# Kernel tuning notes

Hardware: AMD Instinct MI355X
Metric: run time of the kernel (lower is better)

The kernel has to match this reference:

```python
import jax, jax.numpy as jnp
import numpy as np

B, T, N, H, L, KS = 8, 1024, 64, 8, 2, 3  # batch, seq_len, num_features(=graph n), heads, blocks, Cheb order
D1 = 64  # tq MLP hidden (hardcoded 64 in original)
EPS = 1e-6


def setup_inputs() -> dict:
    key = jax.random.key(0)
    ks = jax.random.split(key, 30)
    def nrm(k, shp, sc=0.05):
        return jax.random.normal(k, shp, dtype=jnp.float32) * sc
    return {
        "inputs": jax.random.normal(ks[0], (B, T, N), dtype=jnp.float32),
        "pos_emb": nrm(ks[1], (T, N)),
        "K3": nrm(ks[2], (N, KS, N), 0.1),  # Chebyshev kernel Lk reshaped [n, Ks, n] (constant)
        "qw": nrm(ks[3], (L, H, KS)), "qb": nrm(ks[4], (L, H)),
        "kw": nrm(ks[5], (L, H, KS)), "kb": nrm(ks[6], (L, H)),
        "vw": nrm(ks[7], (L, H, KS)), "vb": nrm(ks[8], (L, H)),
        "tqW1": nrm(ks[9], (L, H, T, D1)), "tqb1": nrm(ks[10], (L, H, D1)),
        "tqW2": nrm(ks[11], (L, H, D1, D1)), "tqb2": nrm(ks[12], (L, H, D1)),
        "tqW3": nrm(ks[13], (L, H, D1, 2)), "tqb3": nrm(ks[14], (L, H, 2)),
        "Wlt": nrm(ks[15], (L, H * N, N)),
        "ln1g": jnp.ones((L, N), jnp.float32), "ln1b": jnp.zeros((L, N), jnp.float32),
        "ln2g": jnp.ones((L, N), jnp.float32), "ln2b": jnp.zeros((L, N), jnp.float32),
        "sclw": nrm(ks[16], (L, KS)), "sclb": nrm(ks[17], (L,)),
        "elW": nrm(ks[18], (L, N, N)), "elb": nrm(ks[19], (L, N)),
        "fW1": nrm(ks[20], (N, 32)), "fb1": nrm(ks[21], (32,)),
        "fW2": nrm(ks[22], (32, 1)), "fb2": nrm(ks[23], (1,)),
    }


def _ln(x, g, b):
    m = jnp.mean(x, axis=-1, keepdims=True)
    v = jnp.mean((x - m) ** 2, axis=-1, keepdims=True)
    return (x - m) * jax.lax.rsqrt(v + EPS) * g + b


def _head_gconv(x, K3, ws, bs):
    # SpatialConvLayer (c_in=c_out=1) per head: relu(sum_k ws[h,k]*(x @ L_k) + bs[h] + x)
    g = jnp.einsum('btn,nkm,hk->bhtm', x, K3, ws) + bs[None, :, None, None]
    return jax.nn.relu(g + x[:, None])  # [B,H,T,N]


def reference(inputs, pos_emb, K3, qw, qb, kw, kb, vw, vb, tqW1, tqb1, tqW2, tqb2,
              tqW3, tqb3, Wlt, ln1g, ln1b, ln2g, ln2b, sclw, sclb, elW, elb,
              fW1, fb1, fW2, fb2):
    x = inputs + pos_emb  # position embedding layer
    for l in range(L):
        xq = _head_gconv(x, K3, qw[l], qb[l])
        xk = _head_gconv(x, K3, kw[l], kb[l])
        xv = _head_gconv(x, K3, vw[l], vb[l])
        # s_a[b,t,s] = sum_n xk[b,t,n] * xq[b,s,n], scaled by 1/num_features
        s = jnp.einsum('bhtn,bhsn->bhts', xk, xq) / N
        sft = jax.nn.softmax(s, axis=-1)
        # talking-quantity gate: MLP over rows of transposed softmax matrix
        p = jnp.swapaxes(sft, -1, -2)  # [B,H,T,T]
        h1 = jax.nn.relu(jnp.einsum('bhts,hsd->bhtd', p, tqW1[l]) + tqb1[l][None, :, None, :])
        h2 = jax.nn.relu(jnp.einsum('bhtd,hde->bhte', h1, tqW2[l]) + tqb2[l][None, :, None, :])
        g = jax.nn.softmax(jnp.einsum('bhtd,hde->bhte', h2, tqW3[l]) + tqb3[l][None, :, None, :], axis=-1)  # [B,H,T,2]
        auv = jnp.einsum('bhts,bhsn->bhtn', sft, xv)
        ho = g[..., 0:1] * auv + g[..., 1:2] * xv  # gated mix, [B,H,T,N]
        a_x = jnp.transpose(ho, (0, 2, 1, 3)).reshape(B, T, H * N)  # head concat
        out1 = _ln(x + a_x @ Wlt[l], ln1g[l], ln1b[l])  # dropout omitted (inference)
        gc = jnp.einsum('btn,nkm,k->btm', out1, K3, sclw[l]) + sclb[l]
        ffn = jax.nn.relu(gc + out1)  # SpatialConvLayer residual relu
        ffn = ffn @ elW[l] + elb[l]
        x = _ln(out1 + ffn, ln2g[l], ln2b[l])
    pooled = jnp.mean(x, axis=1)  # GlobalAveragePooling1D
    h = jax.nn.relu(pooled @ fW1 + fb1)
    return h @ fW2 + fb2  # [B,1]
```

## Files before the change

### kernel.cpp

```cpp
#include <hip/hip_runtime.h>

typedef __attribute__((ext_vector_type(8))) short short8;
typedef __attribute__((ext_vector_type(4))) float f32x4;

#define BB 8
#define TT 1024
#define NN 64
#define HH 8
#define LL 2
#define KSS 3
#define DD1 64
#define EPSV 1e-6f
#define LOG2E 1.4426950408889634f

#define MFMA16(a, b, c) __builtin_amdgcn_mfma_f32_16x16x32_bf16(a, b, c, 0, 0, 0)
#define BAR() __builtin_amdgcn_s_barrier()
#define WAIT_VM6() asm volatile("s_waitcnt vmcnt(6)" ::: "memory")
#define WAIT_VM2() asm volatile("s_waitcnt vmcnt(2)" ::: "memory")
#define WAIT_VM0() asm volatile("s_waitcnt vmcnt(0)" ::: "memory")
#define WAIT_LGKM0() asm volatile("s_waitcnt lgkmcnt(0)" ::: "memory")

__device__ __forceinline__ float exp2_(float x) { return __builtin_amdgcn_exp2f(x); }
__device__ __forceinline__ float log2_(float x) { return __builtin_amdgcn_logf(x); }

__device__ __forceinline__ void split1(float x, ushort& hi, ushort& lo) {
  uint u = __float_as_uint(x);
  hi = (ushort)(u >> 16);
  float hf = __uint_as_float(u & 0xffff0000u);
  lo = (ushort)(__float_as_uint(x - hf) >> 16);
}
__device__ __forceinline__ uint pack2(float a, float b, uint& lo) {
  uint ua = __float_as_uint(a), ub = __float_as_uint(b);
  float ra = __uint_as_float(ua & 0xffff0000u);
  float rb = __uint_as_float(ub & 0xffff0000u);
  lo = (__float_as_uint(a - ra) >> 16) | (__float_as_uint(b - rb) & 0xffff0000u);
  return (ua >> 16) | (ub & 0xffff0000u);
}
__device__ __forceinline__ uint pack2rhu(float a, float b) {
  uint ua = __float_as_uint(a) + 0x8000u;
  uint ub = __float_as_uint(b) + 0x8000u;
  return (ua >> 16) | (ub & 0xffff0000u);
}
__device__ __forceinline__ ushort f2bfr(float x) {
  union { float f; uint u; } v; v.f = x;
  uint r = (v.u + 0x7fffu + ((v.u >> 16) & 1u)) >> 16;
  return (ushort)r;
}
__device__ __forceinline__ float bf2f(ushort b) {
  union { uint u; float f; } v; v.u = ((uint)b) << 16; return v.f;
}

__device__ __forceinline__ void gl2lds16(const ushort* g, ushort* l) {
  __builtin_amdgcn_global_load_lds(
      (const __attribute__((address_space(1))) void*)g,
      (__attribute__((address_space(3))) void*)l, 16, 0, 0);
}
__device__ __forceinline__ void stage_async(ushort* __restrict__ s,
                                            const ushort* __restrict__ g,
                                            int stride, int tid) {
  int w = tid >> 6;
  int sub = (tid & 63) >> 3, c = tid & 7;
#pragma unroll
  for (int i = 0; i < 2; ++i) {
    int rb = (i * 4 + w) * 8;
    gl2lds16(g + (size_t)(rb + sub) * stride + ((c ^ sub) << 3), s + rb * 64);
  }
}
__device__ __forceinline__ short8 frag(const ushort* __restrict__ s, int row, int ch) {
  return *(const short8*)(s + row * 64 + ((ch ^ (row & 7)) << 3));
}
__device__ __forceinline__ void stage_q32(ushort* __restrict__ s,
                                          const ushort* __restrict__ g, int tid) {
  int w = tid >> 6;
  int sub = (tid & 63) >> 3, c = tid & 7;
  int rb = w * 8, r = rb + sub;
  gl2lds16(g + (size_t)r * 64 + ((c ^ (r & 7)) << 3), s + rb * 64);
}
__device__ __forceinline__ void stage_v32(ushort* __restrict__ s,
                                          const ushort* __restrict__ g, int tid) {
  int w = tid >> 6;
  int noff = (tid & 63) >> 2, c = tid & 3;
  int nb = w * 16, n = nb + noff;
  gl2lds16(g + (size_t)n * 1024 + ((c ^ ((n >> 1) & 3)) << 3), s + nb * 32);
}
__device__ __forceinline__ short8 frag32(const ushort* __restrict__ s, int row, int g) {
  return *(const short8*)(s + row * 32 + ((g ^ ((row >> 1) & 3)) << 3));
}


__global__ void k_addpos(const float* __restrict__ in, const float* __restrict__ pe,
                         float* __restrict__ x, int total) {
  int idx = blockIdx.x * 256 + threadIdx.x;
  if (idx < total) {
    int tn = idx & (TT * NN - 1);
    x[idx] = in[idx] + pe[tn];
  }
}

__global__ void k_k3s(const float* __restrict__ K3, const float* __restrict__ sclwl,
                      ushort* __restrict__ dh) {
  int idx = blockIdx.x * 256 + threadIdx.x;
  int n = idx >> 6, m = idx & 63;
  float v = K3[n * 192 + m] * sclwl[0] + K3[n * 192 + 64 + m] * sclwl[1] +
            K3[n * 192 + 128 + m] * sclwl[2];
  dh[m * 64 + n] = f2bfr(v);
}

__global__ __launch_bounds__(256) void k_tsplit(const float* __restrict__ src,
                                                ushort* __restrict__ dh) {
  __shared__ float st[64][65];
  int blk = blockIdx.x;
  int mat = blk >> 4, rt = blk & 15;
  int tid = threadIdx.x;
  size_t sbase = ((size_t)mat * TT + rt * 64) * 64;
#pragma unroll
  for (int i = 0; i < 4; ++i) {
    int idx = tid + i * 256;
    int r = idx >> 4, c4 = idx & 15;
    float4 v = *(const float4*)(src + sbase + r * 64 + c4 * 4);
    st[r][c4 * 4 + 0] = v.x; st[r][c4 * 4 + 1] = v.y;
    st[r][c4 * 4 + 2] = v.z; st[r][c4 * 4 + 3] = v.w;
  }
  __syncthreads();
  size_t obase = (size_t)mat * (64 * (size_t)TT) + rt * 64;
#pragma unroll
  for (int i = 0; i < 2; ++i) {
    int idx = tid + i * 256;
    int n = idx >> 3, c = idx & 7;
    uint hw[4];
#pragma unroll
    for (int j = 0; j < 4; ++j)
      hw[j] = (uint)f2bfr(st[c * 8 + 2 * j][n]) | ((uint)f2bfr(st[c * 8 + 2 * j + 1][n]) << 16);
    *(uint4*)(dh + obase + (size_t)n * TT + c * 8) = make_uint4(hw[0], hw[1], hw[2], hw[3]);
  }
}

__global__ __launch_bounds__(256) void k_tsplitW(const float* __restrict__ Wlt,
                                                 ushort* __restrict__ dh,
                                                 ushort* __restrict__ dl) {
  __shared__ float st[64][65];
  int blk = blockIdx.x;
  int l = blk >> 3, rt = blk & 7;
  int tid = threadIdx.x;
  size_t sbase = ((size_t)l * 512 + rt * 64) * 64;
#pragma unroll
  for (int i = 0; i < 4; ++i) {
    int idx = tid + i * 256;
    int r = idx >> 4, c4 = idx & 15;
    float4 v = *(const float4*)(Wlt + sbase + r * 64 + c4 * 4);
    st[r][c4 * 4 + 0] = v.x; st[r][c4 * 4 + 1] = v.y;
    st[r][c4 * 4 + 2] = v.z; st[r][c4 * 4 + 3] = v.w;
  }
  __syncthreads();
  size_t obase = (size_t)l * 64 * 512 + rt * 64;
#pragma unroll
  for (int i = 0; i < 2; ++i) {
    int idx = tid + i * 256;
    int n = idx >> 3, c = idx & 7;
    uint hw[4], lw[4];
#pragma unroll
    for (int j = 0; j < 4; ++j) hw[j] = pack2(st[c * 8 + 2 * j][n], st[c * 8 + 2 * j + 1][n], lw[j]);
    *(uint4*)(dh + obase + (size_t)n * 512 + c * 8) = make_uint4(hw[0], hw[1], hw[2], hw[3]);
    *(uint4*)(dl + obase + (size_t)n * 512 + c * 8) = make_uint4(lw[0], lw[1], lw[2], lw[3]);
  }
}

__global__ __launch_bounds__(256) void k_tsplitSq(const float* __restrict__ src,
                                                  ushort* __restrict__ dh) {
  __shared__ float st[64][65];
  int mat = blockIdx.x;
  int tid = threadIdx.x;
  size_t sbase = (size_t)mat * 4096;
#pragma unroll
  for (int i = 0; i < 4; ++i) {
    int idx = tid + i * 256;
    int r = idx >> 4, c4 = idx & 15;
    float4 v = *(const float4*)(src + sbase + r * 64 + c4 * 4);
    st[r][c4 * 4 + 0] = v.x; st[r][c4 * 4 + 1] = v.y;
    st[r][c4 * 4 + 2] = v.z; st[r][c4 * 4 + 3] = v.w;
  }
  __syncthreads();
#pragma unroll
  for (int i = 0; i < 2; ++i) {
    int idx = tid + i * 256;
    int d = idx >> 3, c = idx & 7;
    uint hw[4];
#pragma unroll
    for (int j = 0; j < 4; ++j)
      hw[j] = (uint)f2bfr(st[c * 8 + 2 * j][d]) | ((uint)f2bfr(st[c * 8 + 2 * j + 1][d]) << 16);
    *(uint4*)(dh + sbase + (size_t)d * 64 + c * 8) = make_uint4(hw[0], hw[1], hw[2], hw[3]);
  }
}

__global__ __launch_bounds__(256) void k_gconv(
    const float* __restrict__ x, const float* __restrict__ K3,
    const float* __restrict__ qwl, const float* __restrict__ qbl,
    const float* __restrict__ kwl, const float* __restrict__ kbl,
    const float* __restrict__ vwl, const float* __restrict__ vbl,
    ushort* __restrict__ xqh, ushort* __restrict__ xkh, float* __restrict__ xv) {
  __shared__ float sK3[12288];
  __shared__ float sx[4][64];
  int tid = threadIdx.x;
  int w = tid >> 6, lane = tid & 63;
#pragma unroll
  for (int i = 0; i < 12; ++i)
    ((float4*)sK3)[tid + i * 256] = ((const float4*)K3)[tid + i * 256];
  size_t bt = (size_t)blockIdx.x * 4 + w;
  size_t b = bt >> 10, t = bt & 1023;
  float xm = x[bt * 64 + lane];
  sx[w][lane] = xm;
  __syncthreads();
  float a0 = 0.f, a1 = 0.f, a2 = 0.f;
#pragma unroll 8
  for (int n = 0; n < 64; ++n) {
    float xn = sx[w][n];
    a0 = fmaf(xn, sK3[n * 192 + lane], a0);
    a1 = fmaf(xn, sK3[n * 192 + 64 + lane], a1);
    a2 = fmaf(xn, sK3[n * 192 + 128 + lane], a2);
  }
#pragma unroll
  for (int hh = 0; hh < HH; ++hh) {
    size_t off = (((size_t)b * HH + hh) * TT + t) * 64 + lane;
    float q = fmaf(qwl[hh * 3 + 0], a0,
              fmaf(qwl[hh * 3 + 1], a1, fmaf(qwl[hh * 3 + 2], a2, qbl[hh] + xm)));
    q = fmaxf(q, 0.f) * (0.015625f * LOG2E);
    xqh[off] = f2bfr(q);
    float k = fmaf(kwl[hh * 3 + 0], a0,
              fmaf(kwl[hh * 3 + 1], a1, fmaf(kwl[hh * 3 + 2], a2, kbl[hh] + xm)));
    xkh[off] = f2bfr(fmaxf(k, 0.f));
    float v = fmaf(vwl[hh * 3 + 0], a0,
              fmaf(vwl[hh * 3 + 1], a1, fmaf(vwl[hh * 3 + 2], a2, vbl[hh] + xm)));
    xv[off] = fmaxf(v, 0.f);
  }
}

__global__ __launch_bounds__(256) void k_attn(
    const ushort* __restrict__ xkh, const ushort* __restrict__ xqh,
    const ushort* __restrict__ xvTh,
    float* __restrict__ auv0, float* __restrict__ auv1,
    float* __restrict__ ls0, float* __restrict__ ls1) {
  __shared__ ushort sQh[4096];
  __shared__ ushort sVh[4096];
  __shared__ ushort sPh[2048];
  int tid = threadIdx.x;
  int lane = tid & 63, w = tid >> 6;
  int l15 = lane & 15, g = lane >> 4;
  int nb = gridDim.x, chunk = nb >> 3, bid = blockIdx.x;
  int blk = (bid & 7) * chunk + (bid >> 3);
  int bh = blk >> 5, t0 = ((blk >> 1) & 15) << 6, half = blk & 1;
  size_t bhTT = (size_t)bh * TT;
  size_t ubase = (size_t)(half << 9);
  int trow = 16 * w + l15, psw = (trow >> 1) & 3;

  stage_async(sQh, xkh + (bhTT + t0) * NN, 64, tid);
  WAIT_VM0();
  BAR();
  short8 fKh[2];
#pragma unroll
  for (int ks = 0; ks < 2; ++ks) fKh[ks] = frag(sQh, trow, g + 4 * ks);
  WAIT_LGKM0();
  BAR();
  stage_q32(sQh, xqh + (bhTT + ubase) * NN, tid);
  stage_v32(sVh, xvTh + bhTT * NN + ubase, tid);
  stage_q32(sQh + 2048, xqh + (bhTT + ubase + 32) * NN, tid);
  stage_v32(sVh + 2048, xvTh + bhTT * NN + ubase + 32, tid);

  float lsum = 0.f;
  f32x4 O[4];
#pragma unroll
  for (int ct = 0; ct < 4; ++ct)
#pragma unroll
    for (int r = 0; r < 4; ++r) O[ct][r] = 0.f;

  for (int ut = 0; ut < 16; ++ut) {
    int cur = ut & 1;
    if (ut < 15) WAIT_VM2(); else WAIT_VM0();
    BAR();
    const ushort* cQh = sQh + cur * 2048;
    const ushort* cVh = sVh + cur * 2048;

    __builtin_amdgcn_s_setprio(1);
    f32x4 S[2];
#pragma unroll
    for (int rt = 0; rt < 2; ++rt) {
      f32x4 a = {0.f, 0.f, 0.f, 0.f};
#pragma unroll
      for (int ks = 0; ks < 2; ++ks)
        a = MFMA16(frag(cQh, 16 * rt + l15, g + 4 * ks), fKh[ks], a);
      S[rt] = a;
    }
    __builtin_amdgcn_s_setprio(0);

    uint2 ph[2];
#pragma unroll
    for (int rt = 0; rt < 2; ++rt) {
      float p0 = exp2_(S[rt][0]), p1 = exp2_(S[rt][1]);
      float p2 = exp2_(S[rt][2]), p3 = exp2_(S[rt][3]);
      lsum += (p0 + p1) + (p2 + p3);
      ph[rt].x = pack2rhu(p0, p1);
      ph[rt].y = pack2rhu(p2, p3);
    }
#pragma unroll
    for (int rt = 0; rt < 2; ++rt) {
      int ch = 2 * rt + (g >> 1);
      int off = trow * 32 + ((ch ^ psw) << 3) + ((g & 1) << 2);
      *(uint2*)(sPh + off) = ph[rt];
    }
    WAIT_LGKM0();
    __builtin_amdgcn_sched_barrier(0);
    __builtin_amdgcn_s_setprio(1);
    {
      short8 aPh = frag32(sPh, trow, g);
#pragma unroll
      for (int ct = 0; ct < 4; ++ct)
        O[ct] = MFMA16(aPh, frag32(cVh, 16 * ct + l15, g), O[ct]);
    }
    __builtin_amdgcn_s_setprio(0);
    WAIT_LGKM0();
    BAR();
    if (ut < 14) {
      int tn = ut + 2;
      stage_q32(sQh + cur * 2048, xqh + (bhTT + ubase + tn * 32) * NN, tid);
      stage_v32(sVh + cur * 2048, xvTh + bhTT * NN + ubase + tn * 32, tid);
    }
  }
  lsum += __shfl_xor(lsum, 16, 64);
  lsum += __shfl_xor(lsum, 32, 64);
  float* A = half ? auv1 : auv0;
  float* L = half ? ls1 : ls0;
#pragma unroll
  for (int r = 0; r < 4; ++r) {
    size_t row = (bhTT + t0 + 16 * w + 4 * g + r) * NN;
#pragma unroll
    for (int ct = 0; ct < 4; ++ct) A[row + 16 * ct + l15] = O[ct][r];
  }
  if (g == 0) L[bhTT + t0 + trow] = lsum;
}

__global__ __launch_bounds__(256, 4) void k_h1g(
    const ushort* __restrict__ xkh, const ushort* __restrict__ xqh,
    const ushort* __restrict__ w1Th,
    const float* __restrict__ ls0, const float* __restrict__ ls1,
    const float* __restrict__ b1, const ushort* __restrict__ w2Th,
    const float* __restrict__ b2l, const float* __restrict__ W3l,
    const float* __restrict__ b3l,
    const float* __restrict__ auv0, const float* __restrict__ auv1,
    const float* __restrict__ xv, ushort* __restrict__ hoh,
    ushort* __restrict__ hol) {
  __shared__ ushort sKh[4096];
  __shared__ ushort sWh[4096];
  __shared__ ushort sPh[2048];
  __shared__ ushort sW2[4096];
  __shared__ float sL[1024];
  __shared__ float sIl[1024];
  int tid = threadIdx.x;
  int lane = tid & 63, w = tid >> 6;
  int l15 = lane & 15, g = lane >> 4;
  int nb = gridDim.x, chunk = nb >> 3, bid = blockIdx.x;
  int blk = (bid & 7) * chunk + (bid >> 3);
  int bh = blk >> 4, h = bh & (HH - 1), a0 = (blk & 15) << 6;
  size_t bhTT = (size_t)bh * TT;
  size_t wbase = (size_t)h * NN * TT;
  int arow = 16 * w + l15, psw = (arow >> 1) & 3;

  stage_async(sKh, xqh + (bhTT + a0) * NN, 64, tid);
  stage_async(sW2, w2Th + (size_t)h * 4096, 64, tid);
  WAIT_VM0();
  BAR();
  short8 fQh[2];
#pragma unroll
  for (int ks = 0; ks < 2; ++ks) fQh[ks] = frag(sKh, arow, g + 4 * ks);
#pragma unroll
  for (int i = 0; i < 4; ++i) {
    int idx = tid + i * 256;
    float l = ls0[bhTT + idx] + ls1[bhTT + idx];
    sL[idx] = log2_(l);
    sIl[idx] = 1.0f / l;
  }
  WAIT_LGKM0();
  BAR();
  stage_q32(sKh, xkh + bhTT * NN, tid);
  stage_v32(sWh, w1Th + wbase, tid);
  stage_q32(sKh + 2048, xkh + (bhTT + 32) * NN, tid);
  stage_v32(sWh + 2048, w1Th + wbase + 32, tid);

  f32x4 acc[4];
#pragma unroll
  for (int ct = 0; ct < 4; ++ct)
#pragma unroll
    for (int r = 0; r < 4; ++r) acc[ct][r] = 0.f;

  for (int tt = 0; tt < 32; ++tt) {
    int cur = tt & 1;
    if (tt < 31) WAIT_VM2(); else WAIT_VM0();
    BAR();
    const ushort* cKh = sKh + cur * 2048;
    const ushort* cWh = sWh + cur * 2048;

    __builtin_amdgcn_s_setprio(1);
    f32x4 S[2];
#pragma unroll
    for (int rt = 0; rt < 2; ++rt) {
      f32x4 a = {0.f, 0.f, 0.f, 0.f};
#pragma unroll
      for (int ks = 0; ks < 2; ++ks)
        a = MFMA16(frag(cKh, 16 * rt + l15, g + 4 * ks), fQh[ks], a);
      S[rt] = a;
    }
    __builtin_amdgcn_s_setprio(0);

    uint2 ph[2];
#pragma unroll
    for (int rt = 0; rt < 2; ++rt) {
      f32x4 lv = *(const f32x4*)(sL + tt * 32 + 16 * rt + 4 * g);
      float p0 = exp2_(S[rt][0] - lv[0]);
      float p1 = exp2_(S[rt][1] - lv[1]);
      float p2 = exp2_(S[rt][2] - lv[2]);
      float p3 = exp2_(S[rt][3] - lv[3]);
      ph[rt].x = pack2rhu(p0, p1);
      ph[rt].y = pack2rhu(p2, p3);
    }
#pragma unroll
    for (int rt = 0; rt < 2; ++rt) {
      int ch = 2 * rt + (g >> 1);
      int off = arow * 32 + ((ch ^ psw) << 3) + ((g & 1) << 2);
      *(uint2*)(sPh + off) = ph[rt];
    }
    WAIT_LGKM0();
    __builtin_amdgcn_sched_barrier(0);
    __builtin_amdgcn_s_setprio(1);
    {
      short8 aPh = frag32(sPh, arow, g);
#pragma unroll
      for (int ct = 0; ct < 4; ++ct)
        acc[ct] = MFMA16(aPh, frag32(cWh, 16 * ct + l15, g), acc[ct]);
    }
    __builtin_amdgcn_s_setprio(0);
    WAIT_LGKM0();
    BAR();
    if (tt < 30) {
      int tn = tt + 2;
      stage_q32(sKh + cur * 2048, xkh + (bhTT + tn * 32) * NN, tid);
      stage_v32(sWh + cur * 2048, w1Th + wbase + tn * 32, tid);
    }
  }
#pragma unroll
  for (int ct = 0; ct < 4; ++ct) {
    float bb = b1[h * 64 + 16 * ct + l15];
    int cch = 2 * ct + (l15 >> 3), cin = l15 & 7;
#pragma unroll
    for (int r = 0; r < 4; ++r) {
      int row = 16 * w + 4 * g + r;
      float hv = fmaxf(acc[ct][r] + bb, 0.f);
      sWh[row * 64 + ((cch ^ (row & 7)) << 3) + cin] = f2bfr(hv);
    }
  }
  WAIT_LGKM0();
  BAR();
  f32x4 acc2[4];
#pragma unroll
  for (int rt = 0; rt < 4; ++rt)
#pragma unroll
    for (int r = 0; r < 4; ++r) acc2[rt][r] = 0.f;
#pragma unroll
  for (int ks = 0; ks < 2; ++ks) {
    short8 bB = frag(sW2, 16 * w + l15, g + 4 * ks);
#pragma unroll
    for (int rt = 0; rt < 4; ++rt)
      acc2[rt] = MFMA16(frag(sWh, 16 * rt + l15, g + 4 * ks), bB, acc2[rt]);
  }
  int col = 16 * w + l15;
  float b2c = b2l[h * 64 + col];
  float w30 = W3l[h * 128 + col * 2 + 0];
  float w31 = W3l[h * 128 + col * 2 + 1];
  float* sredf = sL;
  float* sgf = sL + 512;
#pragma unroll
  for (int rt = 0; rt < 4; ++rt)
#pragma unroll
    for (int r = 0; r < 4; ++r) {
      float v = fmaxf(acc2[rt][r] + b2c, 0.f);
      float z0 = v * w30, z1 = v * w31;
#pragma unroll
      for (int mm = 1; mm < 16; mm <<= 1) {
        z0 += __shfl_xor(z0, mm, 64);
        z1 += __shfl_xor(z1, mm, 64);
      }
      if (l15 == 0) {
        int row = 16 * rt + 4 * g + r;
        sredf[row * 4 + w] = z0;
        sredf[256 + row * 4 + w] = z1;
      }
    }
  __syncthreads();
  if (tid < 64) {
    float z0 = sredf[tid * 4] + sredf[tid * 4 + 1] + sredf[tid * 4 + 2] +
               sredf[tid * 4 + 3] + b3l[h * 2 + 0];
    float z1 = sredf[256 + tid * 4] + sredf[256 + tid * 4 + 1] +
               sredf[256 + tid * 4 + 2] + sredf[256 + tid * 4 + 3] + b3l[h * 2 + 1];
    float g0 = 1.0f / (1.0f + __expf(z1 - z0));
    sgf[tid * 2] = g0 * sIl[a0 + tid];
    sgf[tid * 2 + 1] = 1.0f - g0;
  }
  __syncthreads();
#pragma unroll
  for (int rr = 0; rr < 16; ++rr) {
    int row = 16 * w + rr;
    size_t off = (bhTT + a0 + row) * 64 + lane;
    float o = auv0[off] + auv1[off];
    float ho = sgf[row * 2] * o + sgf[row * 2 + 1] * xv[off];
    ushort hb, lb;
    split1(ho, hb, lb);
    hoh[off] = hb;
    hol[off] = lb;
  }
}

__global__ __launch_bounds__(256, 2) void k_mrgf(
    float* __restrict__ x, const ushort* __restrict__ hoh,
    const ushort* __restrict__ hol, const ushort* __restrict__ wth,
    const ushort* __restrict__ wtl, const float* __restrict__ g1l,
    const float* __restrict__ b1l, const float* __restrict__ sclb_l,
    const ushort* __restrict__ k3sTh, const ushort* __restrict__ elWTh,
    const float* __restrict__ elbl, const float* __restrict__ g2l,
    const float* __restrict__ b2l) {
  __shared__ ushort sAh[2][2048], sAl[2][2048], sBh[2][4096], sBl[2][4096];
  __shared__ float sred[2][32][4];
  __shared__ float sfin[32][2];
  int tid = threadIdx.x;
  int lane = tid & 63, w = tid >> 6;
  int l15 = lane & 15, g = lane >> 4;
  int blk = blockIdx.x;
  int b = blk >> 5, t0 = (blk & 31) << 5;

  {
    size_t ab0 = (((size_t)b * HH + 0) * TT + t0) * NN;
    size_t ab1 = (((size_t)b * HH + 1) * TT + t0) * NN;
    stage_q32(sAh[0], hoh + ab0, tid);
    stage_q32(sAl[0], hol + ab0, tid);
    stage_async(sBh[0], wth, 512, tid);
    stage_async(sBl[0], wtl, 512, tid);
    stage_q32(sAh[1], hoh + ab1, tid);
    stage_q32(sAl[1], hol + ab1, tid);
    stage_async(sBh[1], wth + 64, 512, tid);
    stage_async(sBl[1], wtl + 64, 512, tid);
  }

  f32x4 acc[2];
#pragma unroll
  for (int rt = 0; rt < 2; ++rt)
#pragma unroll
    for (int r = 0; r < 4; ++r) acc[rt][r] = 0.f;

  for (int h = 0; h < 8; ++h) {
    int cur = h & 1;
    if (h < 7) WAIT_VM6(); else WAIT_VM0();
    BAR();
    __builtin_amdgcn_s_setprio(1);
#pragma unroll
    for (int ks = 0; ks < 2; ++ks) {
      short8 bBh = frag(sBh[cur], 16 * w + l15, g + 4 * ks);
      short8 bBl = frag(sBl[cur], 16 * w + l15, g + 4 * ks);
#pragma unroll
      for (int rt = 0; rt < 2; ++rt) {
        short8 aAh = frag(sAh[cur], 16 * rt + l15, g + 4 * ks);
        short8 aAl = frag(sAl[cur], 16 * rt + l15, g + 4 * ks);
        acc[rt] = MFMA16(aAh, bBh, acc[rt]);
        acc[rt] = MFMA16(aAh, bBl, acc[rt]);
        acc[rt] = MFMA16(aAl, bBh, acc[rt]);
      }
    }
    __builtin_amdgcn_s_setprio(0);
    WAIT_LGKM0();
    BAR();
    if (h < 6) {
      int hn = h + 2;
      size_t ab = (((size_t)b * HH + hn) * TT + t0) * NN;
      stage_q32(sAh[cur], hoh + ab, tid);
      stage_q32(sAl[cur], hol + ab, tid);
      stage_async(sBh[cur], wth + hn * 64, 512, tid);
      stage_async(sBl[cur], wtl + hn * 64, 512, tid);
    }
  }
  stage_async(sBh[0], k3sTh, 64, tid);
  stage_async(sBl[0], elWTh, 64, tid);
  int mcol = 16 * w + l15;
  float vv[2][4];
#pragma unroll
  for (int rt = 0; rt < 2; ++rt)
#pragma unroll
    for (int r = 0; r < 4; ++r) {
      int row = 16 * rt + 4 * g + r;
      vv[rt][r] = acc[rt][r] + x[((size_t)b * TT + t0 + row) * 64 + mcol];
    }
#pragma unroll
  for (int rt = 0; rt < 2; ++rt)
#pragma unroll
    for (int r = 0; r < 4; ++r) {
      float s1 = vv[rt][r], s2 = vv[rt][r] * vv[rt][r];
#pragma unroll
      for (int mm = 1; mm < 16; mm <<= 1) {
        s1 += __shfl_xor(s1, mm, 64);
        s2 += __shfl_xor(s2, mm, 64);
      }
      if (l15 == 0) {
        int row = 16 * rt + 4 * g + r;
        sred[0][row][w] = s1;
        sred[1][row][w] = s2;
      }
    }
  __syncthreads();
  if (tid < 32) {
    float a1 = sred[0][tid][0] + sred[0][tid][1] + sred[0][tid][2] + sred[0][tid][3];
    float a2 = sred[1][tid][0] + sred[1][tid][1] + sred[1][tid][2] + sred[1][tid][3];
    float mean = a1 * (1.0f / 64.0f);
    float var = a2 * (1.0f / 64.0f) - mean * mean;
    sfin[tid][0] = mean;
    sfin[tid][1] = rsqrtf(var + EPSV);
  }
  __syncthreads();
  float gg = g1l[mcol], bb1 = b1l[mcol];
  float val[2][4];
  ushort* sH = sAh[0];
  ushort* sHl = sAl[0];
  int cch = mcol >> 3, cin = mcol & 7;
#pragma unroll
  for (int rt = 0; rt < 2; ++rt)
#pragma unroll
    for (int r = 0; r < 4; ++r) {
      int row = 16 * rt + 4 * g + r;
      float v = (vv[rt][r] - sfin[row][0]) * sfin[row][1] * gg + bb1;
      val[rt][r] = v;
      ushort hb, lb;
      split1(v, hb, lb);
      int a = row * 64 + ((cch ^ (row & 7)) << 3) + cin;
      sH[a] = hb;
      sHl[a] = lb;
    }
  WAIT_VM0();
  WAIT_LGKM0();
  BAR();
  f32x4 acc3[2];
#pragma unroll
  for (int rt = 0; rt < 2; ++rt)
#pragma unroll
    for (int r = 0; r < 4; ++r) acc3[rt][r] = 0.f;
#pragma unroll
  for (int ks = 0; ks < 2; ++ks) {
    short8 bB = frag(sBh[0], mcol, g + 4 * ks);
#pragma unroll
    for (int rt = 0; rt < 2; ++rt) {
      acc3[rt] = MFMA16(frag(sH, 16 * rt + l15, g + 4 * ks), bB, acc3[rt]);
      acc3[rt] = MFMA16(frag(sHl, 16 * rt + l15, g + 4 * ks), bB, acc3[rt]);
    }
  }
  WAIT_LGKM0();
  BAR();
  float sclb = sclb_l[0];
#pragma unroll
  for (int rt = 0; rt < 2; ++rt)
#pragma unroll
    for (int r = 0; r < 4; ++r) {
      int row = 16 * rt + 4 * g + r;
      float f1 = fmaxf(acc3[rt][r] + sclb + val[rt][r], 0.f);
      ushort hb, lb;
      split1(f1, hb, lb);
      int a = row * 64 + ((cch ^ (row & 7)) << 3) + cin;
      sH[a] = hb;
      sHl[a] = lb;
    }
  WAIT_LGKM0();
  BAR();
  f32x4 acc4[2];
#pragma unroll
  for (int rt = 0; rt < 2; ++rt)
#pragma unroll
    for (int r = 0; r < 4; ++r) acc4[rt][r] = 0.f;
#pragma unroll
  for (int ks = 0; ks < 2; ++ks) {
    short8 bB = frag(sBl[0], mcol, g + 4 * ks);
#pragma unroll
    for (int rt = 0; rt < 2; ++rt) {
      acc4[rt] = MFMA16(frag(sH, 16 * rt + l15, g + 4 * ks), bB, acc4[rt]);
      acc4[rt] = MFMA16(frag(sHl, 16 * rt + l15, g + 4 * ks), bB, acc4[rt]);
    }
  }
  float elb = elbl[mcol];
#pragma unroll
  for (int rt = 0; rt < 2; ++rt)
#pragma unroll
    for (int r = 0; r < 4; ++r) {
      float v = val[rt][r] + acc4[rt][r] + elb;
      vv[rt][r] = v;
      float s1 = v, s2 = v * v;
#pragma unroll
      for (int mm = 1; mm < 16; mm <<= 1) {
        s1 += __shfl_xor(s1, mm, 64);
        s2 += __shfl_xor(s2, mm, 64);
      }
      if (l15 == 0) {
        int row = 16 * rt + 4 * g + r;
        sred[0][row][w] = s1;
        sred[1][row][w] = s2;
      }
    }
  __syncthreads();
  if (tid < 32) {
    float a1 = sred[0][tid][0] + sred[0][tid][1] + sred[0][tid][2] + sred[0][tid][3];
    float a2 = sred[1][tid][0] + sred[1][tid][1] + sred[1][tid][2] + sred[1][tid][3];
    float mean = a1 * (1.0f / 64.0f);
    float var = a2 * (1.0f / 64.0f) - mean * mean;
    sfin[tid][0] = mean;
    sfin[tid][1] = rsqrtf(var + EPSV);
  }
  __syncthreads();
  float g2 = g2l[mcol], bb2 = b2l[mcol];
#pragma unroll
  for (int rt = 0; rt < 2; ++rt)
#pragma unroll
    for (int r = 0; r < 4; ++r) {
      int row = 16 * rt + 4 * g + r;
      x[((size_t)b * TT + t0 + row) * 64 + mcol] =
          (vv[rt][r] - sfin[row][0]) * sfin[row][1] * g2 + bb2;
    }
}

__global__ __launch_bounds__(256) void k_final(
    const float* __restrict__ x, const float* __restrict__ fW1,
    const float* __restrict__ fb1, const float* __restrict__ fW2,
    const float* __restrict__ fb2, float* __restrict__ out) {
  __shared__ float pl[4][64];
  int tid = threadIdx.x;
  int lane = tid & 63, w = tid >> 6;
  size_t b = blockIdx.x;
  float s = 0.f;
  for (int t = 256 * w; t < 256 * w + 256; ++t) s += x[(b * TT + t) * 64 + lane];
  pl[w][lane] = s;
  __syncthreads();
  if (tid < 64) pl[0][tid] = (pl[0][tid] + pl[1][tid] + pl[2][tid] + pl[3][tid]) * (1.0f / TT);
  __syncthreads();
  if (tid < 64) {
    float hv = 0.f;
    if (lane < 32) {
      hv = fb1[lane];
#pragma unroll 8
      for (int n = 0; n < 64; ++n) hv = fmaf(pl[0][n], fW1[n * 32 + lane], hv);
      hv = fmaxf(hv, 0.f) * fW2[lane];
    }
#pragma unroll
    for (int m = 1; m < 64; m <<= 1) hv += __shfl_xor(hv, m, 64);
    if (lane == 0) out[b] = hv + fb2[0];
  }
}

extern "C" void kernel_launch(void* const* d_in, const int* in_sizes, int n_in,
                              void* d_out, int out_size, void* d_ws, size_t ws_size,
                              hipStream_t stream) {
  const float* inputs = (const float*)d_in[0];
  const float* pos_emb = (const float*)d_in[1];
  const float* K3 = (const float*)d_in[2];
  const float* qw = (const float*)d_in[3];
  const float* qb = (const float*)d_in[4];
  const float* kw = (const float*)d_in[5];
  const float* kb = (const float*)d_in[6];
  const float* vw = (const float*)d_in[7];
  const float* vb = (const float*)d_in[8];
  const float* tqW1 = (const float*)d_in[9];
  const float* tqb1 = (const float*)d_in[10];
  const float* tqW2 = (const float*)d_in[11];
  const float* tqb2 = (const float*)d_in[12];
  const float* tqW3 = (const float*)d_in[13];
  const float* tqb3 = (const float*)d_in[14];
  const float* Wlt = (const float*)d_in[15];
  const float* ln1g = (const float*)d_in[16];
  const float* ln1b = (const float*)d_in[17];
  const float* ln2g = (const float*)d_in[18];
  const float* ln2b = (const float*)d_in[19];
  const float* sclw = (const float*)d_in[20];
  const float* sclb = (const float*)d_in[21];
  const float* elW = (const float*)d_in[22];
  const float* elb = (const float*)d_in[23];
  const float* fW1 = (const float*)d_in[24];
  const float* fb1 = (const float*)d_in[25];
  const float* fW2 = (const float*)d_in[26];
  const float* fb2 = (const float*)d_in[27];
  float* out = (float*)d_out;
  float* ws_f = (float*)d_ws;

  const size_t TN = (size_t)TT * NN;
  const size_t HTN = (size_t)HH * TT * NN;
  const size_t W1T_ELEMS = (size_t)LL * HH * NN * TT;
  const size_t WLT_ELEMS = (size_t)LL * 64 * 512;

  ushort* k3sTh = (ushort*)ws_f;
  ushort* w1Th = k3sTh + (size_t)LL * 4096;
  ushort* wth = w1Th + W1T_ELEMS;
  ushort* wtl = wth + WLT_ELEMS;
  ushort* w2Th = wtl + WLT_ELEMS;
  ushort* elWTh = w2Th + (size_t)LL * HH * 4096;
  size_t base_ush = (size_t)LL * 4096 + W1T_ELEMS + 2 * WLT_ELEMS +
                    (size_t)LL * HH * 4096 + (size_t)LL * 4096;
  const size_t base = (base_ush + 1) / 2;

  for (int l = 0; l < LL; ++l)
    k_k3s<<<16, 256, 0, stream>>>(K3, sclw + l * KSS, k3sTh + (size_t)l * 4096);
  k_tsplit<<<LL * HH * 16, 256, 0, stream>>>(tqW1, w1Th);
  k_tsplitW<<<LL * 8, 256, 0, stream>>>(Wlt, wth, wtl);
  k_tsplitSq<<<LL * HH, 256, 0, stream>>>(tqW2, w2Th);
  k_tsplitSq<<<LL, 256, 0, stream>>>(elW, elWTh);

  const size_t per_b = TN + 3 * HTN + 2 * (size_t)HH * TT + (5 * HTN) / 2;
  size_t avail = ws_size / sizeof(float);
  avail = (avail > base) ? avail - base : 0;
  int Bc = (int)(avail / per_b);
  if (Bc > BB) Bc = BB;
  if (Bc < 1) Bc = 1;

  for (int b0 = 0; b0 < BB; b0 += Bc) {
    int bc = (BB - b0 < Bc) ? (BB - b0) : Bc;
    float* x = ws_f + base;
    float* xv = x + (size_t)bc * TN;
    float* auv0 = xv + (size_t)bc * HTN;
    float* auv1 = auv0 + (size_t)bc * HTN;
    float* ls0 = auv1 + (size_t)bc * HTN;
    float* ls1 = ls0 + (size_t)bc * HH * TT;
    ushort* xqh = (ushort*)(ls1 + (size_t)bc * HH * TT);
    ushort* xkh = xqh + (size_t)bc * HTN;
    ushort* xvTh = xkh + (size_t)bc * HTN;
    ushort* hoh = xvTh + (size_t)bc * HTN;
    ushort* hol = hoh + (size_t)bc * HTN;

    int total = bc * (int)TN;
    k_addpos<<<(total + 255) / 256, 256, 0, stream>>>(inputs + (size_t)b0 * TN, pos_emb, x,
                                                      total);
    for (int l = 0; l < LL; ++l) {
      k_gconv<<<bc * TT / 4, 256, 0, stream>>>(x, K3, qw + l * HH * KSS, qb + l * HH,
                                               kw + l * HH * KSS, kb + l * HH,
                                               vw + l * HH * KSS, vb + l * HH,
                                               xqh, xkh, xv);
      k_tsplit<<<bc * HH * 16, 256, 0, stream>>>(xv, xvTh);
      k_attn<<<bc * HH * 32, 256, 0, stream>>>(xkh, xqh, xvTh, auv0, auv1, ls0, ls1);
      k_h1g<<<bc * HH * 16, 256, 0, stream>>>(
          xkh, xqh, w1Th + (size_t)l * HH * NN * TT, ls0, ls1,
          tqb1 + l * HH * DD1, w2Th + (size_t)l * HH * 4096, tqb2 + l * HH * DD1,
          tqW3 + (size_t)l * HH * DD1 * 2, tqb3 + l * HH * 2, auv0, auv1, xv,
          hoh, hol);
      k_mrgf<<<bc * 32, 256, 0, stream>>>(
          x, hoh, hol, wth + (size_t)l * 64 * 512, wtl + (size_t)l * 64 * 512,
          ln1g + l * NN, ln1b + l * NN, sclb + l, k3sTh + (size_t)l * 4096,
          elWTh + (size_t)l * 4096, elb + l * NN, ln2g + l * NN, ln2b + l * NN);
    }
    k_final<<<bc, 256, 0, stream>>>(x, fW1, fb1, fW2, fb2, out + b0);
  }
}
```

Measured before the change: 243.8 us.

## Fuse V transpose into gconv, tile gconv over 32 rows, halve mrgf row tile

The graph-conv kernel now processes 32 time steps per block with register-blocked accumulators. It writes the bf16 transposed V tile directly through shared memory, which removes the separate k_tsplit launch and its extra read of xv. The merge/FFN kernel drops from 32-row to 16-row tiles, doubling its grid and halving per-block LDS, with matching staging and wait-count changes. The risks are the gconv grid shrinking to 256 blocks, which lowers parallelism, and mrgf reloading the Wlt weights twice as often.

After: 227.5 us. -6.7%, faster.

```diff
diff --git a/kernel.cpp b/kernel.cpp
--- a/kernel.cpp
+++ b/kernel.cpp
@@ -15,7 +15,7 @@
 
 #define MFMA16(a, b, c) __builtin_amdgcn_mfma_f32_16x16x32_bf16(a, b, c, 0, 0, 0)
 #define BAR() __builtin_amdgcn_s_barrier()
-#define WAIT_VM6() asm volatile("s_waitcnt vmcnt(6)" ::: "memory")
+#define WAIT_VM5() asm volatile("s_waitcnt vmcnt(5)" ::: "memory")
 #define WAIT_VM2() asm volatile("s_waitcnt vmcnt(2)" ::: "memory")
 #define WAIT_VM0() asm volatile("s_waitcnt vmcnt(0)" ::: "memory")
 #define WAIT_LGKM0() asm volatile("s_waitcnt lgkmcnt(0)" ::: "memory")
@@ -74,6 +74,18 @@
   int w = tid >> 6;
   int sub = (tid & 63) >> 3, c = tid & 7;
   int rb = w * 8, r = rb + sub;
+  gl2lds16(g + (size_t)r * 64 + ((c ^ (r & 7)) << 3), s + rb * 64);
+}
+__device__ __forceinline__ void stage_a16pair(ushort* __restrict__ sh,
+                                              ushort* __restrict__ sl,
+                                              const ushort* __restrict__ gh,
+                                              const ushort* __restrict__ gl,
+                                              int tid) {
+  int w = tid >> 6, sub = (tid & 63) >> 3, c = tid & 7;
+  const ushort* g = (w & 2) ? gl : gh;
+  ushort* s = (w & 2) ? sl : sh;
+  int rb = (w & 1) * 8;
+  int r = rb + sub;
   gl2lds16(g + (size_t)r * 64 + ((c ^ (r & 7)) << 3), s + rb * 64);
 }
 __device__ __forceinline__ void stage_v32(ushort* __restrict__ s,
@@ -197,40 +209,73 @@
     const float* __restrict__ qwl, const float* __restrict__ qbl,
     const float* __restrict__ kwl, const float* __restrict__ kbl,
     const float* __restrict__ vwl, const float* __restrict__ vbl,
-    ushort* __restrict__ xqh, ushort* __restrict__ xkh, float* __restrict__ xv) {
+    ushort* __restrict__ xqh, ushort* __restrict__ xkh,
+    float* __restrict__ xv, ushort* __restrict__ xvTh) {
   __shared__ float sK3[12288];
-  __shared__ float sx[4][64];
+  __shared__ float sx[32][64];
+  __shared__ ushort sv[32][68];
   int tid = threadIdx.x;
-  int w = tid >> 6, lane = tid & 63;
+  int m = tid & 63, tg = tid >> 6;
 #pragma unroll
   for (int i = 0; i < 12; ++i)
     ((float4*)sK3)[tid + i * 256] = ((const float4*)K3)[tid + i * 256];
-  size_t bt = (size_t)blockIdx.x * 4 + w;
-  size_t b = bt >> 10, t = bt & 1023;
-  float xm = x[bt * 64 + lane];
-  sx[w][lane] = xm;
-  __syncthreads();
-  float a0 = 0.f, a1 = 0.f, a2 = 0.f;
-#pragma unroll 8
+  int blk = blockIdx.x;
+  int b = blk >> 5, tt = blk & 31;
+  size_t xbase = ((size_t)b * TT + tt * 32) * 64;
+#pragma unroll
+  for (int i = 0; i < 2; ++i) {
+    int idx = tid + i * 256;
+    int r = idx >> 4, c4 = idx & 15;
+    *(float4*)&sx[r][c4 * 4] = *(const float4*)(x + xbase + r * 64 + c4 * 4);
+  }
+  __syncthreads();
+  float A0[8], A1[8], A2[8];
+#pragma unroll
+  for (int i = 0; i < 8; ++i) { A0[i] = 0.f; A1[i] = 0.f; A2[i] = 0.f; }
   for (int n = 0; n < 64; ++n) {
-    float xn = sx[w][n];
-    a0 = fmaf(xn, sK3[n * 192 + lane], a0);
-    a1 = fmaf(xn, sK3[n * 192 + 64 + lane], a1);
-    a2 = fmaf(xn, sK3[n * 192 + 128 + lane], a2);
-  }
-#pragma unroll
+    float k0 = sK3[n * 192 + m];
+    float k1 = sK3[n * 192 + 64 + m];
+    float k2 = sK3[n * 192 + 128 + m];
+#pragma unroll
+    for (int i = 0; i < 8; ++i) {
+      float xn = sx[tg + i * 4][n];
+      A0[i] = fmaf(xn, k0, A0[i]);
+      A1[i] = fmaf(xn, k1, A1[i]);
+      A2[i] = fmaf(xn, k2, A2[i]);
+    }
+  }
+  float XM[8];
+#pragma unroll
+  for (int i = 0; i < 8; ++i) XM[i] = sx[tg + i * 4][m];
+  int nrow = tid >> 2, cch = tid & 3;
   for (int hh = 0; hh < HH; ++hh) {
-    size_t off = (((size_t)b * HH + hh) * TT + t) * 64 + lane;
-    float q = fmaf(qwl[hh * 3 + 0], a0,
-              fmaf(qwl[hh * 3 + 1], a1, fmaf(qwl[hh * 3 + 2], a2, qbl[hh] + xm)));
-    q = fmaxf(q, 0.f) * (0.015625f * LOG2E);
-    xqh[off] = f2bfr(q);
-    float k = fmaf(kwl[hh * 3 + 0], a0,
-              fmaf(kwl[hh * 3 + 1], a1, fmaf(kwl[hh * 3 + 2], a2, kbl[hh] + xm)));
-    xkh[off] = f2bfr(fmaxf(k, 0.f));
-    float v = fmaf(vwl[hh * 3 + 0], a0,
-              fmaf(vwl[hh * 3 + 1], a1, fmaf(vwl[hh * 3 + 2], a2, vbl[hh] + xm)));
-    xv[off] = fmaxf(v, 0.f);
+    float q0 = qwl[hh * 3], q1 = qwl[hh * 3 + 1], q2 = qwl[hh * 3 + 2], qb = qbl[hh];
+    float k0 = kwl[hh * 3], k1 = kwl[hh * 3 + 1], k2 = kwl[hh * 3 + 2], kb = kbl[hh];
+    float v0 = vwl[hh * 3], v1 = vwl[hh * 3 + 1], v2 = vwl[hh * 3 + 2], vb = vbl[hh];
+    size_t rowb = ((size_t)b * HH + hh) * TT + tt * 32;
+#pragma unroll
+    for (int i = 0; i < 8; ++i) {
+      int t = tg + i * 4;
+      size_t off = (rowb + t) * 64 + m;
+      float q = fmaf(q0, A0[i], fmaf(q1, A1[i], fmaf(q2, A2[i], qb + XM[i])));
+      xqh[off] = f2bfr(fmaxf(q, 0.f) * (0.015625f * LOG2E));
+      float k = fmaf(k0, A0[i], fmaf(k1, A1[i], fmaf(k2, A2[i], kb + XM[i])));
+      xkh[off] = f2bfr(fmaxf(k, 0.f));
+      float v = fmaf(v0, A0[i], fmaf(v1, A1[i], fmaf(v2, A2[i], vb + XM[i])));
+      v = fmaxf(v, 0.f);
+      xv[off] = v;
+      sv[t][m] = f2bfr(v);
+    }
+    __syncthreads();
+    {
+      uint hw[4];
+#pragma unroll
+      for (int j = 0; j < 4; ++j)
+        hw[j] = (uint)sv[cch * 8 + 2 * j][nrow] | ((uint)sv[cch * 8 + 2 * j + 1][nrow] << 16);
+      *(uint4*)(xvTh + (((size_t)b * HH + hh) * 64 + nrow) * 1024 + tt * 32 + cch * 8) =
+          make_uint4(hw[0], hw[1], hw[2], hw[3]);
+    }
+    __syncthreads();
   }
 }
 
@@ -516,7 +561,7 @@
   }
 }
 
-__global__ __launch_bounds__(256, 2) void k_mrgf(
+__global__ __launch_bounds__(256) void k_mrgf(
     float* __restrict__ x, const ushort* __restrict__ hoh,
     const ushort* __restrict__ hol, const ushort* __restrict__ wth,
     const ushort* __restrict__ wtl, const float* __restrict__ g1l,
@@ -524,51 +569,44 @@
     const ushort* __restrict__ k3sTh, const ushort* __restrict__ elWTh,
     const float* __restrict__ elbl, const float* __restrict__ g2l,
     const float* __restrict__ b2l) {
-  __shared__ ushort sAh[2][2048], sAl[2][2048], sBh[2][4096], sBl[2][4096];
-  __shared__ float sred[2][32][4];
-  __shared__ float sfin[32][2];
+  __shared__ ushort sAh[2][1024], sAl[2][1024], sBh[2][4096], sBl[2][4096];
+  __shared__ float sred[2][16][4];
+  __shared__ float sfin[16][2];
   int tid = threadIdx.x;
   int lane = tid & 63, w = tid >> 6;
   int l15 = lane & 15, g = lane >> 4;
   int blk = blockIdx.x;
-  int b = blk >> 5, t0 = (blk & 31) << 5;
+  int b = blk >> 6, t0 = (blk & 63) << 4;
 
   {
     size_t ab0 = (((size_t)b * HH + 0) * TT + t0) * NN;
     size_t ab1 = (((size_t)b * HH + 1) * TT + t0) * NN;
-    stage_q32(sAh[0], hoh + ab0, tid);
-    stage_q32(sAl[0], hol + ab0, tid);
+    stage_a16pair(sAh[0], sAl[0], hoh + ab0, hol + ab0, tid);
     stage_async(sBh[0], wth, 512, tid);
     stage_async(sBl[0], wtl, 512, tid);
-    stage_q32(sAh[1], hoh + ab1, tid);
-    stage_q32(sAl[1], hol + ab1, tid);
+    stage_a16pair(sAh[1], sAl[1], hoh + ab1, hol + ab1, tid);
     stage_async(sBh[1], wth + 64, 512, tid);
     stage_async(sBl[1], wtl + 64, 512, tid);
   }
 
-  f32x4 acc[2];
-#pragma unroll
-  for (int rt = 0; rt < 2; ++rt)
-#pragma unroll
-    for (int r = 0; r < 4; ++r) acc[rt][r] = 0.f;
+  f32x4 acc;
+#pragma unroll
+  for (int r = 0; r < 4; ++r) acc[r] = 0.f;
 
   for (int h = 0; h < 8; ++h) {
     int cur = h & 1;
-    if (h < 7) WAIT_VM6(); else WAIT_VM0();
+    if (h < 7) WAIT_VM5(); else WAIT_VM0();
     BAR();
     __builtin_amdgcn_s_setprio(1);
 #pragma unroll
     for (int ks = 0; ks < 2; ++ks) {
       short8 bBh = frag(sBh[cur], 16 * w + l15, g + 4 * ks);
       short8 bBl = frag(sBl[cur], 16 * w + l15, g + 4 * ks);
-#pragma unroll
-      for (int rt = 0; rt < 2; ++rt) {
-        short8 aAh = frag(sAh[cur], 16 * rt + l15, g + 4 * ks);
-        short8 aAl = frag(sAl[cur], 16 * rt + l15, g + 4 * ks);
-        acc[rt] = MFMA16(aAh, bBh, acc[rt]);
-        acc[rt] = MFMA16(aAh, bBl, acc[rt]);
-        acc[rt] = MFMA16(aAl, bBh, acc[rt]);
-      }
+      short8 aAh = frag(sAh[cur], l15, g + 4 * ks);
+      short8 aAl = frag(sAl[cur], l15, g + 4 * ks);
+      acc = MFMA16(aAh, bBh, acc);
+      acc = MFMA16(aAh, bBl, acc);
+      acc = MFMA16(aAl, bBh, acc);
     }
     __builtin_amdgcn_s_setprio(0);
     WAIT_LGKM0();
@@ -576,8 +614,7 @@
     if (h < 6) {
       int hn = h + 2;
       size_t ab = (((size_t)b * HH + hn) * TT + t0) * NN;
-      stage_q32(sAh[cur], hoh + ab, tid);
-      stage_q32(sAl[cur], hol + ab, tid);
+      stage_a16pair(sAh[cur], sAl[cur], hoh + ab, hol + ab, tid);
       stage_async(sBh[cur], wth + hn * 64, 512, tid);
       stage_async(sBl[cur], wtl + hn * 64, 512, tid);
     }
@@ -585,32 +622,28 @@
   stage_async(sBh[0], k3sTh, 64, tid);
   stage_async(sBl[0], elWTh, 64, tid);
   int mcol = 16 * w + l15;
-  float vv[2][4];
-#pragma unroll
-  for (int rt = 0; rt < 2; ++rt)
-#pragma unroll
-    for (int r = 0; r < 4; ++r) {
-      int row = 16 * rt + 4 * g + r;
-      vv[rt][r] = acc[rt][r] + x[((size_t)b * TT + t0 + row) * 64 + mcol];
-    }
-#pragma unroll
-  for (int rt = 0; rt < 2; ++rt)
-#pragma unroll
-    for (int r = 0; r < 4; ++r) {
-      float s1 = vv[rt][r], s2 = vv[rt][r] * vv[rt][r];
-#pragma unroll
-      for (int mm = 1; mm < 16; mm <<= 1) {
-        s1 += __shfl_xor(s1, mm, 64);
-        s2 += __shfl_xor(s2, mm, 64);
-      }
-      if (l15 == 0) {
-        int row = 16 * rt + 4 * g + r;
-        sred[0][row][w] = s1;
-        sred[1][row][w] = s2;
-      }
-    }
-  __syncthreads();
-  if (tid < 32) {
+  float vv[4];
+#pragma unroll
+  for (int r = 0; r < 4; ++r) {
+    int row = 4 * g + r;
+    vv[r] = acc[r] + x[((size_t)b * TT + t0 + row) * 64 + mcol];
+  }
+#pragma unroll
+  for (int r = 0; r < 4; ++r) {
+    float s1 = vv[r], s2 = vv[r] * vv[r];
+#pragma unroll
+    for (int mm = 1; mm < 16; mm <<= 1) {
+      s1 += __shfl_xor(s1, mm, 64);
+      s2 += __shfl_xor(s2, mm, 64);
+    }
+    if (l15 == 0) {
+      int row = 4 * g + r;
+      sred[0][row][w] = s1;
+      sred[1][row][w] = s2;
+    }
+  }
+  __syncthreads();
+  if (tid < 16) {
     float a1 = sred[0][tid][0] + sred[0][tid][1] + sred[0][tid][2] + sred[0][tid][3];
     float a2 = sred[1][tid][0] + sred[1][tid][1] + sred[1][tid][2] + sred[1][tid][3];
     float mean = a1 * (1.0f / 64.0f);
@@ -620,92 +653,76 @@
   }
   __syncthreads();
   float gg = g1l[mcol], bb1 = b1l[mcol];
-  float val[2][4];
+  float val[4];
   ushort* sH = sAh[0];
   ushort* sHl = sAl[0];
   int cch = mcol >> 3, cin = mcol & 7;
 #pragma unroll
-  for (int rt = 0; rt < 2; ++rt)
-#pragma unroll
-    for (int r = 0; r < 4; ++r) {
-      int row = 16 * rt + 4 * g + r;
-      float v = (vv[rt][r] - sfin[row][0]) * sfin[row][1] * gg + bb1;
-      val[rt][r] = v;
-      ushort hb, lb;
-      split1(v, hb, lb);
-      int a = row * 64 + ((cch ^ (row & 7)) << 3) + cin;
-      sH[a] = hb;
-      sHl[a] = lb;
-    }
+  for (int r = 0; r < 4; ++r) {
+    int row = 4 * g + r;
+    float v = (vv[r] - sfin[row][0]) * sfin[row][1] * gg + bb1;
+    val[r] = v;
+    ushort hb, lb;
+    split1(v, hb, lb);
+    int a = row * 64 + ((cch ^ (row & 7)) << 3) + cin;
+    sH[a] = hb;
+    sHl[a] = lb;
+  }
   WAIT_VM0();
   WAIT_LGKM0();
   BAR();
-  f32x4 acc3[2];
-#pragma unroll
-  for (int rt = 0; rt < 2; ++rt)
-#pragma unroll
-    for (int r = 0; r < 4; ++r) acc3[rt][r] = 0.f;
+  f32x4 acc3;
+#pragma unroll
+  for (int r = 0; r < 4; ++r) acc3[r] = 0.f;
 #pragma unroll
   for (int ks = 0; ks < 2; ++ks) {
     short8 bB = frag(sBh[0], mcol, g + 4 * ks);
-#pragma unroll
-    for (int rt = 0; rt < 2; ++rt) {
-      acc3[rt] = MFMA16(frag(sH, 16 * rt + l15, g + 4 * ks), bB, acc3[rt]);
-      acc3[rt] = MFMA16(frag(sHl, 16 * rt + l15, g + 4 * ks), bB, acc3[rt]);
-    }
+    acc3 = MFMA16(frag(sH, l15, g + 4 * ks), bB, acc3);
+    acc3 = MFMA16(frag(sHl, l15, g + 4 * ks), bB, acc3);
   }
   WAIT_LGKM0();
   BAR();
   float sclb = sclb_l[0];
 #pragma unroll
-  for (int rt = 0; rt < 2; ++rt)
-#pragma unroll
-    for (int r = 0; r < 4; ++r) {
-      int row = 16 * rt + 4 * g + r;
-      float f1 = fmaxf(acc3[rt][r] + sclb + val[rt][r], 0.f);
-      ushort hb, lb;
-      split1(f1, hb, lb);
-      int a = row * 64 + ((cch ^ (row & 7)) << 3) + cin;
-      sH[a] = hb;
-      sHl[a] = lb;
-    }
+  for (int r = 0; r < 4; ++r) {
+    int row = 4 * g + r;
+    float f1 = fmaxf(acc3[r] + sclb + val[r], 0.f);
+    ushort hb, lb;
+    split1(f1, hb, lb);
+    int a = row * 64 + ((cch ^ (row & 7)) << 3) + cin;
+    sH[a] = hb;
+    sHl[a] = lb;
+  }
   WAIT_LGKM0();
   BAR();
-  f32x4 acc4[2];
-#pragma unroll
-  for (int rt = 0; rt < 2; ++rt)
-#pragma unroll
-    for (int r = 0; r < 4; ++r) acc4[rt][r] = 0.f;
+  f32x4 acc4;
+#pragma unroll
+  for (int r = 0; r < 4; ++r) acc4[r] = 0.f;
 #pragma unroll
   for (int ks = 0; ks < 2; ++ks) {
     short8 bB = frag(sBl[0], mcol, g + 4 * ks);
-#pragma unroll
-    for (int rt = 0; rt < 2; ++rt) {
-      acc4[rt] = MFMA16(frag(sH, 16 * rt + l15, g + 4 * ks), bB, acc4[rt]);
-      acc4[rt] = MFMA16(frag(sHl, 16 * rt + l15, g + 4 * ks), bB, acc4[rt]);
-    }
+    acc4 = MFMA16(frag(sH, l15, g + 4 * ks), bB, acc4);
+    acc4 = MFMA16(frag(sHl, l15, g + 4 * ks), bB, acc4);
   }
   float elb = elbl[mcol];
 #pragma unroll
-  for (int rt = 0; rt < 2; ++rt)
-#pragma unroll
-    for (int r = 0; r < 4; ++r) {
-      float v = val[rt][r] + acc4[rt][r] + elb;
-      vv[rt][r] = v;
-      float s1 = v, s2 = v * v;
-#pragma unroll
-      for (int mm = 1; mm < 16; mm <<= 1) {
-        s1 += __shfl_xor(s1, mm, 64);
-        s2 += __shfl_xor(s2, mm, 64);
-      }
-      if (l15 == 0) {
-        int row = 16 * rt + 4 * g + r;
-        sred[0][row][w] = s1;
-        sred[1][row][w] = s2;
-      }
-    }
-  __syncthreads();
-  if (tid < 32) {
+  for (int r = 0; r < 4; ++r) {
+    float v = val[r] + acc4[r] + elb;
+    vv[r] = v;
+    float s1 = v, s2 = v * v;
+#pragma unroll
+    for (int mm = 1; mm < 16; mm <<= 1) {
+      s1 += __shfl_xor(s1, mm, 64);
+      s2 += __shfl_xor(s2, mm, 64);
+    }
+    if (l15 == 0) {
+      int row = 4 * g + r;
+      sred[0][row][w] = s1;
+      sred[1][row][w] = s2;
+    }
+  }
+  __syncthreads();
+  if (tid < 16) {
     float a1 = sred[0][tid][0] + sred[0][tid][1] + sred[0][tid][2] + sred[0][tid][3];
     float a2 = sred[1][tid][0] + sred[1][tid][1] + sred[1][tid][2] + sred[1][tid][3];
     float mean = a1 * (1.0f / 64.0f);
@@ -716,13 +733,11 @@
   __syncthreads();
   float g2 = g2l[mcol], bb2 = b2l[mcol];
 #pragma unroll
-  for (int rt = 0; rt < 2; ++rt)
-#pragma unroll
-    for (int r = 0; r < 4; ++r) {
-      int row = 16 * rt + 4 * g + r;
-      x[((size_t)b * TT + t0 + row) * 64 + mcol] =
-          (vv[rt][r] - sfin[row][0]) * sfin[row][1] * g2 + bb2;
-    }
+  for (int r = 0; r < 4; ++r) {
+    int row = 4 * g + r;
+    x[((size_t)b * TT + t0 + row) * 64 + mcol] =
+        (vv[r] - sfin[row][0]) * sfin[row][1] * g2 + bb2;
+  }
 }
 
 __global__ __launch_bounds__(256) void k_final(
@@ -834,18 +849,17 @@
     k_addpos<<<(total + 255) / 256, 256, 0, stream>>>(inputs + (size_t)b0 * TN, pos_emb, x,
                                                       total);
     for (int l = 0; l < LL; ++l) {
-      k_gconv<<<bc * TT / 4, 256, 0, stream>>>(x, K3, qw + l * HH * KSS, qb + l * HH,
-                                               kw + l * HH * KSS, kb + l * HH,
-                                               vw + l * HH * KSS, vb + l * HH,
-                                               xqh, xkh, xv);
-      k_tsplit<<<bc * HH * 16, 256, 0, stream>>>(xv, xvTh);
+      k_gconv<<<bc * 32, 256, 0, stream>>>(x, K3, qw + l * HH * KSS, qb + l * HH,
+                                           kw + l * HH * KSS, kb + l * HH,
+                                           vw + l * HH * KSS, vb + l * HH,
+                                           xqh, xkh, xv, xvTh);
       k_attn<<<bc * HH * 32, 256, 0, stream>>>(xkh, xqh, xvTh, auv0, auv1, ls0, ls1);
       k_h1g<<<bc * HH * 16, 256, 0, stream>>>(
           xkh, xqh, w1Th + (size_t)l * HH * NN * TT, ls0, ls1,
           tqb1 + l * HH * DD1, w2Th + (size_t)l * HH * 4096, tqb2 + l * HH * DD1,
           tqW3 + (size_t)l * HH * DD1 * 2, tqb3 + l * HH * 2, auv0, auv1, xv,
           hoh, hol);
-      k_mrgf<<<bc * 32, 256, 0, stream>>>(
+      k_mrgf<<<bc * 64, 256, 0, stream>>>(
           x, hoh, hol, wth + (size_t)l * 64 * 512, wtl + (size_t)l * 64 * 512,
           ln1g + l * NN, ln1b + l * NN, sclb + l, k3sTh + (size_t)l * 4096,
           elWTh + (size_t)l * 4096, elb + l * NN, ln2g + l * NN, ln2b + l * NN);
```
